# Kernel optimization log

Measured on AMD Instinct MI355X. Metric: run time of the kernel, lower is better.

The kernel has to match this reference:

```python
import jax, jax.numpy as jnp
import numpy as np

DT_SCALER = 1.0 / 24.0
ODE_STEPS = 4  # fixed-step RK4 stand-in for adaptive odeint(rtol=atol=1e-3)
B, T, D, H = 1024, 100, 32, 256
ODE_MID = 50  # hidden width of the ODE func MLP (hard-coded 50 in source)


def setup_inputs() -> dict:
    key = jax.random.key(0)
    ks = jax.random.split(key, 20)
    n = lambda k, s: jax.random.normal(k, s, dtype=jnp.float32)
    std = 0.1  # module inits weights N(0, 0.1), biases 0
    return {
        "dt": jax.random.uniform(ks[0], (B, T, 2), dtype=jnp.float32),
        "x": n(ks[1], (B, T, D)),
        # RNNCell params
        "W_ih": n(ks[2], (H, D)) * std,
        "b_ih": jnp.zeros((H,), jnp.float32),
        "W_hh": n(ks[3], (H, H)) * std,
        "b_hh": jnp.zeros((H,), jnp.float32),
        # ODE func: Linear(H,50) -> tanh -> Linear(50,H)
        "ode_w1": n(ks[4], (ODE_MID, H)) * std,
        "ode_b1": jnp.zeros((ODE_MID,), jnp.float32),
        "ode_w2": n(ks[5], (H, ODE_MID)) * std,
        "ode_b2": jnp.zeros((H,), jnp.float32),
        # mu head: l1 (H -> H//2), distribution_mu (H//2 -> 1)
        "l1_w": n(ks[6], (H // 2, H)) * std,
        "l1_b": jnp.zeros((H // 2,), jnp.float32),
        "mu_w": n(ks[7], (1, H // 2)) * std,
        "mu_b": jnp.zeros((1,), jnp.float32),
        # sigma head: Linear(H,H) -> tanh -> Linear(H,1) -> softplus
        "sig_w1": n(ks[8], (H, H)) * std,
        "sig_b1": jnp.zeros((H,), jnp.float32),
        "sig_w2": n(ks[9], (1, H)) * std,
        "sig_b2": jnp.zeros((1,), jnp.float32),
    }


def reference(dt, x, W_ih, b_ih, W_hh, b_hh, ode_w1, ode_b1, ode_w2, ode_b2,
              l1_w, l1_b, mu_w, mu_b, sig_w1, sig_b1, sig_w2, sig_b2):
    Bsz = x.shape[0]
    xs = jnp.swapaxes(x, 0, 1)                               # [T,B,D]
    dts = jnp.swapaxes(dt[:, :, 1] - dt[:, :, 0], 0, 1)[..., None]  # [T,B,1]
    h0 = jnp.zeros((Bsz, W_hh.shape[0]), x.dtype)
    hs = 1.0 / ODE_STEPS

    def ode_f(y, scale):
        # net(y) * (dt * DT_SCALER); RHS is time-independent
        return (jnp.tanh(y @ ode_w1.T + ode_b1) @ ode_w2.T + ode_b2) * scale

    def step(h, inp):
        x_i, dt_i = inp                                      # [B,D], [B,1]
        # h_t = h_t + RNNCell(x_i, h_t)
        h = h + jnp.tanh(x_i @ W_ih.T + b_ih + h @ W_hh.T + b_hh)
        scale = dt_i * DT_SCALER
        # integrate dh/dt = ode_f(h) from t=0 to t=1 (fixed-step RK4)
        def rk4(y, _):
            k1 = ode_f(y, scale)
            k2 = ode_f(y + 0.5 * hs * k1, scale)
            k3 = ode_f(y + 0.5 * hs * k2, scale)
            k4 = ode_f(y + hs * k3, scale)
            return y + (hs / 6.0) * (k1 + 2.0 * k2 + 2.0 * k3 + k4), None
        h, _ = jax.lax.scan(rk4, h, None, length=ODE_STEPS)
        # heads (eval mode: dropout is identity)
        mu = jax.nn.relu(h @ l1_w.T + l1_b) @ mu_w.T + mu_b              # [B,1]
        sig = jax.nn.softplus(jnp.tanh(h @ sig_w1.T + sig_b1) @ sig_w2.T + sig_b2)
        return h, (mu, sig)

    _, (mu_seq, sig_seq) = jax.lax.scan(step, h0, (xs, dts))
    mu_out = jnp.swapaxes(mu_seq, 0, 1)    # [B,T,1]
    sig_out = jnp.swapaxes(sig_seq, 0, 1)  # [B,T,1]
    return (mu_out, sig_out)
```

## Files before the change

kernel.cpp:

```cpp
#include <hip/hip_runtime.h>
#include <math.h>


#define NT 256

#define WS_WCAT 0
#define WS_L1P  73728
#define WS_SW1  106496
#define WS_TOT  172032

#define F4_YC   0
#define F4_MID  256
#define F4_PRR  320
#define F4_PH1  320
#define F4_PH2  1376
#define F4_XS   2416
#define F4_L1O  2448
#define F4_SG   2576
#define F4_W1   2832
#define F4_W2   6160
#define F4_END  9488
#define SM_BC   (F4_END*4)
#define SM_OB2  (SM_BC+256)
#define SM_L1B  (SM_OB2+256)
#define SM_SB1  (SM_L1B+128)
#define SM_MUW  (SM_SB1+256)
#define SM_SW2  (SM_MUW+128)
#define SM_SCL  (SM_SW2+256)
#define SM_TOTF (SM_SCL+4)
#define SMEM_BYTES (SM_TOTF*4)

__device__ __forceinline__ float fma4(float a, float4 y, float4 w) {
  a = fmaf(y.x, w.x, a); a = fmaf(y.y, w.y, a);
  a = fmaf(y.z, w.z, a); a = fmaf(y.w, w.w, a);
  return a;
}
__device__ __forceinline__ float4 add4(float4 a, float4 b) {
  return make_float4(a.x+b.x, a.y+b.y, a.z+b.z, a.w+b.w);
}
__device__ __forceinline__ float4 axpy4(float a, float4 xv, float4 yv) {
  return make_float4(fmaf(a,xv.x,yv.x), fmaf(a,xv.y,yv.y),
                     fmaf(a,xv.z,yv.z), fmaf(a,xv.w,yv.w));
}
__device__ __forceinline__ float4 muls4(float4 v, float s) {
  return make_float4(v.x*s, v.y*s, v.z*s, v.w*s);
}
__device__ __forceinline__ float tfast(float x) {
  float ax = fabsf(x);
  float e  = __expf(-2.f * ax);
  float t  = (1.f - e) * __builtin_amdgcn_rcpf(1.f + e);
  return copysignf(t, x);
}
__device__ __forceinline__ float4 tfast4(float4 v) {
  return make_float4(tfast(v.x), tfast(v.y), tfast(v.z), tfast(v.w));
}
template <int CTRL>
__device__ __forceinline__ float dpp_add(float v) {
  int s = __builtin_amdgcn_update_dpp(0, __float_as_int(v), CTRL, 0xF, 0xF, true);
  return v + __int_as_float(s);
}
__device__ __forceinline__ float red16(float v) {
  return dpp_add<0xB1>(dpp_add<0x4E>(dpp_add<0x141>(dpp_add<0x140>(v))));
}

__global__ void prep_w(const float* __restrict__ Wih, const float* __restrict__ Whh,
                       const float* __restrict__ l1w, const float* __restrict__ sw1,
                       float* __restrict__ ws) {
  int i = blockIdx.x * 256 + threadIdx.x;
  if (i < 73728) {
    int g = i >> 10, rem = i & 1023, j = rem >> 2, c = rem & 3;
    int k = 4 * g + c;
    ws[i] = (k < 32) ? Wih[j * 32 + k] : Whh[j * 256 + (k - 32)];
  } else if (i < 106496) {
    int t = i - 73728;
    int g = t >> 9, rem = t & 511, j = rem >> 2, c = rem & 3;
    ws[i] = l1w[j * 256 + 4 * g + c];
  } else if (i < WS_TOT) {
    int t = i - 106496;
    int g = t >> 10, rem = t & 1023, j = rem >> 2, c = rem & 3;
    ws[i] = sw1[j * 256 + 4 * g + c];
  }
}

__global__ __attribute__((amdgpu_flat_work_group_size(NT, NT)))
void odernn_main(const float* __restrict__ dt,
                 const float* __restrict__ x,
                 const float* __restrict__ bih,
                 const float* __restrict__ bhh,
                 const float* __restrict__ ow1,
                 const float* __restrict__ ob1g,
                 const float* __restrict__ ow2,
                 const float* __restrict__ ob2g,
                 const float* __restrict__ l1bg,
                 const float* __restrict__ muwg,
                 const float* __restrict__ mubg,
                 const float* __restrict__ sb1g,
                 const float* __restrict__ sw2g,
                 const float* __restrict__ sb2g,
                 const float* __restrict__ ws,
                 float* __restrict__ out) {
  extern __shared__ __align__(16) float sm[];
  float4* f4 = (float4*)sm;
  float* midS = sm + F4_MID * 4;
  const int tid = threadIdx.x;
  const int wv = tid >> 6, ln = tid & 63;
  const int b0 = blockIdx.x * 4;
  const bool isA = (wv & 1) == 0;
  const int ra = (wv >> 1) * 2, rb = ra + 1;

  const float4* wcat4 = (const float4*)(ws + WS_WCAT);
  const float4* l1w4  = (const float4*)(ws + WS_L1P);
  const float4* sw14  = (const float4*)(ws + WS_SW1);
  const float4* xg4   = (const float4*)x;

  for (int i = tid; i < 3328; i += NT) {
    int j = i >> 6, rem = i & 63, f = rem >> 4, kq = rem & 15;
    float4 v = make_float4(0.f, 0.f, 0.f, 0.f);
    if (j < 50) v = *(const float4*)&ow1[j * 256 + kq * 16 + 4 * f];
    f4[F4_W1 + (j * 4 + f) * 16 + kq] = v;
  }
  for (int i = tid; i < 3328; i += NT) {
    int cg = i >> 6, lq = i & 63;
    int C = cg / 13, g = cg - C * 13;
    int col = 4 * lq + C;
    float t0 = (4*g+0 < 50) ? ow2[col*50 + 4*g+0] : 0.f;
    float t1 = (4*g+1 < 50) ? ow2[col*50 + 4*g+1] : 0.f;
    float t2 = (4*g+2 < 50) ? ow2[col*50 + 4*g+2] : 0.f;
    float t3 = (4*g+3 < 50) ? ow2[col*50 + 4*g+3] : 0.f;
    f4[F4_W2 + i] = make_float4(t0, t1, t2, t3);
  }
  sm[SM_BC + tid]  = bih[tid] + bhh[tid];
  sm[SM_OB2 + tid] = ob2g[tid];
  sm[SM_SB1 + tid] = sb1g[tid];
  sm[SM_SW2 + tid] = sw2g[tid];
  if (tid < 128) { sm[SM_L1B + tid] = l1bg[tid]; sm[SM_MUW + tid] = muwg[tid]; }
  f4[F4_YC + tid] = make_float4(0.f, 0.f, 0.f, 0.f);
  if (tid < 32) {
    int r = tid >> 3, g = tid & 7;
    f4[F4_XS + tid] = xg4[((size_t)(b0 + r) * 100) * 8 + g];
  } else if (tid < 36) {
    int r = tid - 32;
    const float* dp = dt + ((size_t)(b0 + r) * 100) * 2;
    sm[SM_SCL + r] = (dp[1] - dp[0]) * (1.f / 24.f);
  }
  __syncthreads();

  const float mubv = mubg[0], sb2v = sb2g[0];
  const float4* bc4  = (const float4*)(sm + SM_BC);
  const float4* l1b4 = (const float4*)(sm + SM_L1B);
  const float4* sb14 = (const float4*)(sm + SM_SB1);
  const float4* muw4 = (const float4*)(sm + SM_MUW);
  const float4* sw24 = (const float4*)(sm + SM_SW2);

  auto RNNPART = [&]() {
    const int jq = tid & 63, kc = tid >> 6;
    float4 a0 = make_float4(0,0,0,0), a1 = a0, a2 = a0, a3 = a0;
#pragma unroll 2
    for (int gg = 0; gg < 18; ++gg) {
      int g = kc * 18 + gg;
      float4 w0 = wcat4[g * 256 + 4 * jq + 0];
      float4 w1 = wcat4[g * 256 + 4 * jq + 1];
      float4 w2 = wcat4[g * 256 + 4 * jq + 2];
      float4 w3 = wcat4[g * 256 + 4 * jq + 3];
      float4 y0 = (g < 8) ? f4[F4_XS + g]      : f4[F4_YC + (g - 8)];
      float4 y1 = (g < 8) ? f4[F4_XS + 8 + g]  : f4[F4_YC + 64 + (g - 8)];
      float4 y2 = (g < 8) ? f4[F4_XS + 16 + g] : f4[F4_YC + 128 + (g - 8)];
      float4 y3 = (g < 8) ? f4[F4_XS + 24 + g] : f4[F4_YC + 192 + (g - 8)];
      a0.x = fma4(a0.x, y0, w0); a0.y = fma4(a0.y, y0, w1);
      a0.z = fma4(a0.z, y0, w2); a0.w = fma4(a0.w, y0, w3);
      a1.x = fma4(a1.x, y1, w0); a1.y = fma4(a1.y, y1, w1);
      a1.z = fma4(a1.z, y1, w2); a1.w = fma4(a1.w, y1, w3);
      a2.x = fma4(a2.x, y2, w0); a2.y = fma4(a2.y, y2, w1);
      a2.z = fma4(a2.z, y2, w2); a2.w = fma4(a2.w, y2, w3);
      a3.x = fma4(a3.x, y3, w0); a3.y = fma4(a3.y, y3, w1);
      a3.z = fma4(a3.z, y3, w2); a3.w = fma4(a3.w, y3, w3);
    }
    f4[F4_PRR + (kc * 4 + 0) * 65 + jq] = a0;
    f4[F4_PRR + (kc * 4 + 1) * 65 + jq] = a1;
    f4[F4_PRR + (kc * 4 + 2) * 65 + jq] = a2;
    f4[F4_PRR + (kc * 4 + 3) * 65 + jq] = a3;
  };
  auto RNNRED = [&]() {
    const int r = tid >> 6, jq = tid & 63;
    float4 v = bc4[jq];
#pragma unroll
    for (int kc = 0; kc < 4; ++kc)
      v = add4(v, f4[F4_PRR + (kc * 4 + r) * 65 + jq]);
    float4 hold = f4[F4_YC + r * 64 + jq];
    f4[F4_YC + r * 64 + jq] = add4(hold, tfast4(v));
  };
  auto HEADSPART = [&]() {
    {
      const int cq = tid & 31, kc = tid >> 5;
      float4 c0 = make_float4(0,0,0,0), c1 = c0, c2 = c0, c3 = c0;
#pragma unroll 2
      for (int g = 0; g < 8; ++g) {
        int kg = kc * 8 + g;
        float4 w0 = l1w4[kg * 128 + 4 * cq + 0];
        float4 w1 = l1w4[kg * 128 + 4 * cq + 1];
        float4 w2 = l1w4[kg * 128 + 4 * cq + 2];
        float4 w3 = l1w4[kg * 128 + 4 * cq + 3];
        float4 y0 = f4[F4_YC + kg],       y1 = f4[F4_YC + 64 + kg];
        float4 y2 = f4[F4_YC + 128 + kg], y3 = f4[F4_YC + 192 + kg];
        c0.x = fma4(c0.x, y0, w0); c0.y = fma4(c0.y, y0, w1);
        c0.z = fma4(c0.z, y0, w2); c0.w = fma4(c0.w, y0, w3);
        c1.x = fma4(c1.x, y1, w0); c1.y = fma4(c1.y, y1, w1);
        c1.z = fma4(c1.z, y1, w2); c1.w = fma4(c1.w, y1, w3);
        c2.x = fma4(c2.x, y2, w0); c2.y = fma4(c2.y, y2, w1);
        c2.z = fma4(c2.z, y2, w2); c2.w = fma4(c2.w, y2, w3);
        c3.x = fma4(c3.x, y3, w0); c3.y = fma4(c3.y, y3, w1);
        c3.z = fma4(c3.z, y3, w2); c3.w = fma4(c3.w, y3, w3);
      }
      f4[F4_PH1 + (kc * 4 + 0) * 33 + cq] = c0;
      f4[F4_PH1 + (kc * 4 + 1) * 33 + cq] = c1;
      f4[F4_PH1 + (kc * 4 + 2) * 33 + cq] = c2;
      f4[F4_PH1 + (kc * 4 + 3) * 33 + cq] = c3;
    }
    {
      const int cq = tid & 63, kc = tid >> 6;
      float4 d0 = make_float4(0,0,0,0), d1 = d0, d2 = d0, d3 = d0;
#pragma unroll 2
      for (int g = 0; g < 16; ++g) {
        int kg = kc * 16 + g;
        float4 w0 = sw14[kg * 256 + 4 * cq + 0];
        float4 w1 = sw14[kg * 256 + 4 * cq + 1];
        float4 w2 = sw14[kg * 256 + 4 * cq + 2];
        float4 w3 = sw14[kg * 256 + 4 * cq + 3];
        float4 y0 = f4[F4_YC + kg],       y1 = f4[F4_YC + 64 + kg];
        float4 y2 = f4[F4_YC + 128 + kg], y3 = f4[F4_YC + 192 + kg];
        d0.x = fma4(d0.x, y0, w0); d0.y = fma4(d0.y, y0, w1);
        d0.z = fma4(d0.z, y0, w2); d0.w = fma4(d0.w, y0, w3);
        d1.x = fma4(d1.x, y1, w0); d1.y = fma4(d1.y, y1, w1);
        d1.z = fma4(d1.z, y1, w2); d1.w = fma4(d1.w, y1, w3);
        d2.x = fma4(d2.x, y2, w0); d2.y = fma4(d2.y, y2, w1);
        d2.z = fma4(d2.z, y2, w2); d2.w = fma4(d2.w, y2, w3);
        d3.x = fma4(d3.x, y3, w0); d3.y = fma4(d3.y, y3, w1);
        d3.z = fma4(d3.z, y3, w2); d3.w = fma4(d3.w, y3, w3);
      }
      f4[F4_PH2 + (kc * 4 + 0) * 65 + cq] = d0;
      f4[F4_PH2 + (kc * 4 + 1) * 65 + cq] = d1;
      f4[F4_PH2 + (kc * 4 + 2) * 65 + cq] = d2;
      f4[F4_PH2 + (kc * 4 + 3) * 65 + cq] = d3;
    }
  };
  auto HEADSRED = [&]() {
    if (tid < 128) {
      int r = tid >> 5, cq = tid & 31;
      float4 v = l1b4[cq];
#pragma unroll
      for (int kc = 0; kc < 8; ++kc)
        v = add4(v, f4[F4_PH1 + (kc * 4 + r) * 33 + cq]);
      f4[F4_L1O + r * 32 + cq] =
          make_float4(fmaxf(v.x, 0.f), fmaxf(v.y, 0.f),
                      fmaxf(v.z, 0.f), fmaxf(v.w, 0.f));
    }
    {
      int r = tid >> 6, cq = tid & 63;
      float4 v = sb14[cq];
#pragma unroll
      for (int kc = 0; kc < 4; ++kc)
        v = add4(v, f4[F4_PH2 + (kc * 4 + r) * 65 + cq]);
      f4[F4_SG + r * 64 + cq] = tfast4(v);
    }
  };
  auto DOTS = [&](int t) {
    float pm = 0.f;
    if (ln < 32) {
      float4 l = f4[F4_L1O + wv * 32 + ln];
      float4 w = muw4[ln];
      pm = l.x * w.x + l.y * w.y + l.z * w.z + l.w * w.w;
    }
#pragma unroll
    for (int off = 32; off > 0; off >>= 1) pm += __shfl_down(pm, off);
    if (ln == 0) out[(size_t)(b0 + wv) * 100 + t] = pm + mubv;
    float4 sv = f4[F4_SG + wv * 64 + ln];
    float4 w2v = sw24[ln];
    float ps = sv.x * w2v.x + sv.y * w2v.y + sv.z * w2v.z + sv.w * w2v.w;
#pragma unroll
    for (int off = 32; off > 0; off >>= 1) ps += __shfl_down(ps, off);
    if (ln == 0) {
      float z = ps + sb2v;
      float sp = fmaxf(z, 0.f) + log1pf(expf(-fabsf(z)));
      out[(size_t)102400 + (size_t)(b0 + wv) * 100 + t] = sp;
    }
  };

  if (isA) {
    const int qA = ln >> 4, kcA = ln & 15;
    float4 w1r[13][4];
    float ob1A = 0.f;
    {
      int jb = qA * 13 + kcA;
      if (kcA < 13 && jb < 50) ob1A = ob1g[jb];
    }
    auto L1 = [&](int row) {
      const float4* ycr = f4 + F4_YC + row * 64 + kcA * 4;
      float4 y0 = ycr[0], y1 = ycr[1], y2 = ycr[2], y3 = ycr[3];
      float p[13];
#pragma unroll
      for (int jj = 0; jj < 13; ++jj) {
        float s = 0.f;
        s = fma4(s, y0, w1r[jj][0]); s = fma4(s, y1, w1r[jj][1]);
        s = fma4(s, y2, w1r[jj][2]); s = fma4(s, y3, w1r[jj][3]);
        p[jj] = s;
      }
#pragma unroll
      for (int jj = 0; jj < 13; ++jj) p[jj] = red16(p[jj]);
      if (kcA < 13) {
        float v = p[0];
#pragma unroll
        for (int jj = 1; jj < 13; ++jj) v = (kcA == jj) ? p[jj] : v;
        midS[row * 64 + qA * 13 + kcA] = tfast(v + ob1A);
      }
    };

    for (int t = 0; t < 100; ++t) {
      RNNPART();  __syncthreads();
      RNNRED();   __syncthreads();
#pragma unroll
      for (int jj = 0; jj < 13; ++jj)
#pragma unroll
        for (int f = 0; f < 4; ++f)
          w1r[jj][f] = f4[F4_W1 + ((qA * 13 + jj) * 4 + f) * 16 + kcA];
#pragma unroll 1
      for (int ph = 0; ph <= 32; ++ph) {
        if (ph < 32) {
          L1(ra + (ph & 1));
        } else if (t < 99 && wv == 0) {
          if (ln < 32) {
            int r = ln >> 3, g = ln & 7;
            f4[F4_XS + ln] = xg4[((size_t)(b0 + r) * 100 + t + 1) * 8 + g];
          } else if (ln < 36) {
            int r = ln - 32;
            const float* dp = dt + ((size_t)(b0 + r) * 100 + t + 1) * 2;
            sm[SM_SCL + r] = (dp[1] - dp[0]) * (1.f / 24.f);
          }
        }
        __syncthreads();
      }
      HEADSPART(); __syncthreads();
      HEADSRED();  __syncthreads();
      DOTS(t);     __syncthreads();
    }
  } else {
    float4 w2c0[13], w2c1[13], w2c2[13], w2c3[13];
    float4 hA, hB, acA, acB;
    float sclA = 0.f, sclB = 0.f;
    auto L2 = [&](int row, int e, float4& h, float4& ac, float sc) {
      const float4* mr = (const float4*)(midS + row * 64);
      float bx = 0.f, by = 0.f, bz = 0.f, bw = 0.f;
#define L2STEP(mv, g) bx = fma4(bx, mv, w2c0[g]); by = fma4(by, mv, w2c1[g]); \
                      bz = fma4(bz, mv, w2c2[g]); bw = fma4(bw, mv, w2c3[g]);
      {
        float4 a0 = mr[0], a1 = mr[1], a2 = mr[2], a3 = mr[3], a4 = mr[4];
        L2STEP(a0, 0) L2STEP(a1, 1) L2STEP(a2, 2) L2STEP(a3, 3) L2STEP(a4, 4)
      }
      {
        float4 a0 = mr[5], a1 = mr[6], a2 = mr[7], a3 = mr[8];
        L2STEP(a0, 5) L2STEP(a1, 6) L2STEP(a2, 7) L2STEP(a3, 8)
      }
      {
        float4 a0 = mr[9], a1 = mr[10], a2 = mr[11], a3 = mr[12];
        L2STEP(a0, 9) L2STEP(a1, 10) L2STEP(a2, 11) L2STEP(a3, 12)
      }
#undef L2STEP
      float4 ob2v = ((const float4*)(sm + SM_OB2))[ln];
      float4 kv = muls4(add4(make_float4(bx, by, bz, bw), ob2v), sc);
      const int s = e & 3;
      float4 ycw;
      if (s == 0)      { ac = kv;                 ycw = axpy4(0.125f, kv, h); }
      else if (s == 1) { ac = axpy4(2.f, kv, ac); ycw = axpy4(0.125f, kv, h); }
      else if (s == 2) { ac = axpy4(2.f, kv, ac); ycw = axpy4(0.25f,  kv, h); }
      else             { h = axpy4(0.25f / 6.f, add4(ac, kv), h); ycw = h; }
      f4[F4_YC + row * 64 + ln] = ycw;
    };

    for (int t = 0; t < 100; ++t) {
      RNNPART();  __syncthreads();
      RNNRED();   __syncthreads();
#pragma unroll
      for (int g = 0; g < 13; ++g) {
        w2c0[g] = f4[F4_W2 + (0 * 13 + g) * 64 + ln];
        w2c1[g] = f4[F4_W2 + (1 * 13 + g) * 64 + ln];
        w2c2[g] = f4[F4_W2 + (2 * 13 + g) * 64 + ln];
        w2c3[g] = f4[F4_W2 + (3 * 13 + g) * 64 + ln];
      }
#pragma unroll 1
      for (int ph = 0; ph <= 32; ++ph) {
        if (ph == 0) {
          hA = f4[F4_YC + ra * 64 + ln];
          hB = f4[F4_YC + rb * 64 + ln];
          acA = make_float4(0.f, 0.f, 0.f, 0.f); acB = acA;
          sclA = sm[SM_SCL + ra]; sclB = sm[SM_SCL + rb];
        } else if (ph & 1) {
          L2(ra, (ph - 1) >> 1, hA, acA, sclA);
        } else {
          L2(rb, (ph - 2) >> 1, hB, acB, sclB);
        }
        __syncthreads();
      }
      HEADSPART(); __syncthreads();
      HEADSRED();  __syncthreads();
      DOTS(t);     __syncthreads();
    }
  }
}

extern "C" void kernel_launch(void* const* d_in, const int* in_sizes, int n_in,
                              void* d_out, int out_size, void* d_ws, size_t ws_size,
                              hipStream_t stream) {
  const float* dt  = (const float*)d_in[0];
  const float* x   = (const float*)d_in[1];
  const float* Wih = (const float*)d_in[2];
  const float* bih = (const float*)d_in[3];
  const float* Whh = (const float*)d_in[4];
  const float* bhh = (const float*)d_in[5];
  const float* ow1 = (const float*)d_in[6];
  const float* ob1 = (const float*)d_in[7];
  const float* ow2 = (const float*)d_in[8];
  const float* ob2 = (const float*)d_in[9];
  const float* l1w = (const float*)d_in[10];
  const float* l1b = (const float*)d_in[11];
  const float* muw = (const float*)d_in[12];
  const float* mub = (const float*)d_in[13];
  const float* sw1 = (const float*)d_in[14];
  const float* sb1 = (const float*)d_in[15];
  const float* sw2 = (const float*)d_in[16];
  const float* sb2 = (const float*)d_in[17];
  float* ws  = (float*)d_ws;
  float* out = (float*)d_out;

  hipFuncSetAttribute((const void*)odernn_main,
                      hipFuncAttributeMaxDynamicSharedMemorySize, SMEM_BYTES);

  prep_w<<<WS_TOT / 256, 256, 0, stream>>>(Wih, Whh, l1w, sw1, ws);
  odernn_main<<<256, NT, SMEM_BYTES, stream>>>(dt, x, bih, bhh, ow1, ob1, ow2, ob2,
                                               l1b, muw, mub, sb1, sw2, sb2, ws, out);
}
```

Before: 3.323 ms.

## Run ODE RK4 per-wave per-row without block barriers, keep W1 in registers

Drops the wave-specialized A/B split, where some waves did layer 1 and others did layer 2 with a block barrier per phase. Now each wave integrates its own batch row through all 16 RK4 stages, using only intra-wave LDS communication, so the ~33 __syncthreads per timestep go away. W1 stays in registers for the whole kernel. Intermediate state is stored in a swizzled LDS layout to avoid bank conflicts, and W2 is read from LDS on every stage. The risks are higher register pressure (waves_per_eu(1)), more LDS reads of W2, and each wave now doing both matmuls serially.

```diff
diff --git a/kernel.cpp b/kernel.cpp
--- a/kernel.cpp
+++ b/kernel.cpp
@@ -9,20 +9,19 @@
 #define WS_SW1  106496
 #define WS_TOT  172032
 
-#define F4_YC   0
-#define F4_MID  256
-#define F4_PRR  320
-#define F4_PH1  320
-#define F4_PH2  1376
-#define F4_XS   2416
-#define F4_L1O  2448
-#define F4_SG   2576
-#define F4_W1   2832
-#define F4_W2   6160
-#define F4_END  9488
+#define F4_YCT  0
+#define F4_HS   256
+#define F4_MID  512
+#define F4_PRR  576
+#define F4_PH1  576
+#define F4_PH2  1632
+#define F4_XS   2672
+#define F4_L1O  2704
+#define F4_SG   2832
+#define F4_W2   3088
+#define F4_END  6416
 #define SM_BC   (F4_END*4)
-#define SM_OB2  (SM_BC+256)
-#define SM_L1B  (SM_OB2+256)
+#define SM_L1B  (SM_BC+256)
 #define SM_SB1  (SM_L1B+128)
 #define SM_MUW  (SM_SB1+256)
 #define SM_SW2  (SM_MUW+128)
@@ -61,6 +60,9 @@
 }
 __device__ __forceinline__ float red16(float v) {
   return dpp_add<0xB1>(dpp_add<0x4E>(dpp_add<0x141>(dpp_add<0x140>(v))));
+}
+__device__ __forceinline__ int ycphys(int a) {
+  return ((a & 3) << 4) + ((a >> 2) ^ (a & 3));
 }
 
 __global__ void prep_w(const float* __restrict__ Wih, const float* __restrict__ Whh,
@@ -83,6 +85,7 @@
 }
 
 __global__ __attribute__((amdgpu_flat_work_group_size(NT, NT)))
+__attribute__((amdgpu_waves_per_eu(1)))
 void odernn_main(const float* __restrict__ dt,
                  const float* __restrict__ x,
                  const float* __restrict__ bih,
@@ -105,20 +108,27 @@
   const int tid = threadIdx.x;
   const int wv = tid >> 6, ln = tid & 63;
   const int b0 = blockIdx.x * 4;
-  const bool isA = (wv & 1) == 0;
-  const int ra = (wv >> 1) * 2, rb = ra + 1;
 
   const float4* wcat4 = (const float4*)(ws + WS_WCAT);
   const float4* l1w4  = (const float4*)(ws + WS_L1P);
   const float4* sw14  = (const float4*)(ws + WS_SW1);
   const float4* xg4   = (const float4*)x;
 
-  for (int i = tid; i < 3328; i += NT) {
-    int j = i >> 6, rem = i & 63, f = rem >> 4, kq = rem & 15;
-    float4 v = make_float4(0.f, 0.f, 0.f, 0.f);
-    if (j < 50) v = *(const float4*)&ow1[j * 256 + kq * 16 + 4 * f];
-    f4[F4_W1 + (j * 4 + f) * 16 + kq] = v;
-  }
+  const int qA = ln >> 4, kcA = ln & 15;
+  float4 w1r[13][4];
+  float  ob1r[13];
+#pragma unroll
+  for (int jj = 0; jj < 13; ++jj) {
+    int j = qA * 13 + jj;
+    ob1r[jj] = (j < 50) ? ob1g[j] : 0.f;
+#pragma unroll
+    for (int f = 0; f < 4; ++f)
+      w1r[jj][f] = (j < 50)
+          ? *(const float4*)&ow1[j * 256 + kcA * 16 + 4 * f]
+          : make_float4(0.f, 0.f, 0.f, 0.f);
+  }
+  float4 ob2r = *(const float4*)&ob2g[4 * ln];
+
   for (int i = tid; i < 3328; i += NT) {
     int cg = i >> 6, lq = i & 63;
     int C = cg / 13, g = cg - C * 13;
@@ -129,12 +139,11 @@
     float t3 = (4*g+3 < 50) ? ow2[col*50 + 4*g+3] : 0.f;
     f4[F4_W2 + i] = make_float4(t0, t1, t2, t3);
   }
-  sm[SM_BC + tid]  = bih[tid] + bhh[tid];
-  sm[SM_OB2 + tid] = ob2g[tid];
+  sm[SM_BC + tid] = bih[tid] + bhh[tid];
   sm[SM_SB1 + tid] = sb1g[tid];
   sm[SM_SW2 + tid] = sw2g[tid];
   if (tid < 128) { sm[SM_L1B + tid] = l1bg[tid]; sm[SM_MUW + tid] = muwg[tid]; }
-  f4[F4_YC + tid] = make_float4(0.f, 0.f, 0.f, 0.f);
+  f4[F4_HS + tid] = make_float4(0.f, 0.f, 0.f, 0.f);
   if (tid < 32) {
     int r = tid >> 3, g = tid & 7;
     f4[F4_XS + tid] = xg4[((size_t)(b0 + r) * 100) * 8 + g];
@@ -151,45 +160,94 @@
   const float4* sb14 = (const float4*)(sm + SM_SB1);
   const float4* muw4 = (const float4*)(sm + SM_MUW);
   const float4* sw24 = (const float4*)(sm + SM_SW2);
-
-  auto RNNPART = [&]() {
-    const int jq = tid & 63, kc = tid >> 6;
-    float4 a0 = make_float4(0,0,0,0), a1 = a0, a2 = a0, a3 = a0;
+  const float4* mid4 = (const float4*)midS;
+
+  const int physW = ycphys(ln);
+  const int rowb = wv * 64;
+
+  for (int t = 0; t < 100; ++t) {
+    {
+      const int jq = tid & 63, kc = tid >> 6;
+      float4 a0 = make_float4(0,0,0,0), a1 = a0, a2 = a0, a3 = a0;
 #pragma unroll 2
-    for (int gg = 0; gg < 18; ++gg) {
-      int g = kc * 18 + gg;
-      float4 w0 = wcat4[g * 256 + 4 * jq + 0];
-      float4 w1 = wcat4[g * 256 + 4 * jq + 1];
-      float4 w2 = wcat4[g * 256 + 4 * jq + 2];
-      float4 w3 = wcat4[g * 256 + 4 * jq + 3];
-      float4 y0 = (g < 8) ? f4[F4_XS + g]      : f4[F4_YC + (g - 8)];
-      float4 y1 = (g < 8) ? f4[F4_XS + 8 + g]  : f4[F4_YC + 64 + (g - 8)];
-      float4 y2 = (g < 8) ? f4[F4_XS + 16 + g] : f4[F4_YC + 128 + (g - 8)];
-      float4 y3 = (g < 8) ? f4[F4_XS + 24 + g] : f4[F4_YC + 192 + (g - 8)];
-      a0.x = fma4(a0.x, y0, w0); a0.y = fma4(a0.y, y0, w1);
-      a0.z = fma4(a0.z, y0, w2); a0.w = fma4(a0.w, y0, w3);
-      a1.x = fma4(a1.x, y1, w0); a1.y = fma4(a1.y, y1, w1);
-      a1.z = fma4(a1.z, y1, w2); a1.w = fma4(a1.w, y1, w3);
-      a2.x = fma4(a2.x, y2, w0); a2.y = fma4(a2.y, y2, w1);
-      a2.z = fma4(a2.z, y2, w2); a2.w = fma4(a2.w, y2, w3);
-      a3.x = fma4(a3.x, y3, w0); a3.y = fma4(a3.y, y3, w1);
-      a3.z = fma4(a3.z, y3, w2); a3.w = fma4(a3.w, y3, w3);
-    }
-    f4[F4_PRR + (kc * 4 + 0) * 65 + jq] = a0;
-    f4[F4_PRR + (kc * 4 + 1) * 65 + jq] = a1;
-    f4[F4_PRR + (kc * 4 + 2) * 65 + jq] = a2;
-    f4[F4_PRR + (kc * 4 + 3) * 65 + jq] = a3;
-  };
-  auto RNNRED = [&]() {
-    const int r = tid >> 6, jq = tid & 63;
-    float4 v = bc4[jq];
-#pragma unroll
-    for (int kc = 0; kc < 4; ++kc)
-      v = add4(v, f4[F4_PRR + (kc * 4 + r) * 65 + jq]);
-    float4 hold = f4[F4_YC + r * 64 + jq];
-    f4[F4_YC + r * 64 + jq] = add4(hold, tfast4(v));
-  };
-  auto HEADSPART = [&]() {
+      for (int gg = 0; gg < 18; ++gg) {
+        int g = kc * 18 + gg;
+        float4 w0 = wcat4[g * 256 + 4 * jq + 0];
+        float4 w1 = wcat4[g * 256 + 4 * jq + 1];
+        float4 w2 = wcat4[g * 256 + 4 * jq + 2];
+        float4 w3 = wcat4[g * 256 + 4 * jq + 3];
+        float4 y0 = (g < 8) ? f4[F4_XS + g]      : f4[F4_HS + (g - 8)];
+        float4 y1 = (g < 8) ? f4[F4_XS + 8 + g]  : f4[F4_HS + 64 + (g - 8)];
+        float4 y2 = (g < 8) ? f4[F4_XS + 16 + g] : f4[F4_HS + 128 + (g - 8)];
+        float4 y3 = (g < 8) ? f4[F4_XS + 24 + g] : f4[F4_HS + 192 + (g - 8)];
+        a0.x = fma4(a0.x, y0, w0); a0.y = fma4(a0.y, y0, w1);
+        a0.z = fma4(a0.z, y0, w2); a0.w = fma4(a0.w, y0, w3);
+        a1.x = fma4(a1.x, y1, w0); a1.y = fma4(a1.y, y1, w1);
+        a1.z = fma4(a1.z, y1, w2); a1.w = fma4(a1.w, y1, w3);
+        a2.x = fma4(a2.x, y2, w0); a2.y = fma4(a2.y, y2, w1);
+        a2.z = fma4(a2.z, y2, w2); a2.w = fma4(a2.w, y2, w3);
+        a3.x = fma4(a3.x, y3, w0); a3.y = fma4(a3.y, y3, w1);
+        a3.z = fma4(a3.z, y3, w2); a3.w = fma4(a3.w, y3, w3);
+      }
+      f4[F4_PRR + (kc * 4 + 0) * 65 + jq] = a0;
+      f4[F4_PRR + (kc * 4 + 1) * 65 + jq] = a1;
+      f4[F4_PRR + (kc * 4 + 2) * 65 + jq] = a2;
+      f4[F4_PRR + (kc * 4 + 3) * 65 + jq] = a3;
+    }
+    __syncthreads();
+    float4 h;
+    {
+      float4 v = bc4[ln];
+#pragma unroll
+      for (int kc = 0; kc < 4; ++kc)
+        v = add4(v, f4[F4_PRR + (kc * 4 + wv) * 65 + ln]);
+      h = add4(f4[F4_HS + rowb + ln], tfast4(v));
+      f4[F4_YCT + rowb + physW] = h;
+    }
+    float4 ac = make_float4(0.f, 0.f, 0.f, 0.f);
+    const float sc = sm[SM_SCL + wv];
+#pragma unroll 1
+    for (int e = 0; e < 16; ++e) {
+      float4 y0 = f4[F4_YCT + rowb + 0 * 16 + (kcA ^ 0)];
+      float4 y1 = f4[F4_YCT + rowb + 1 * 16 + (kcA ^ 1)];
+      float4 y2 = f4[F4_YCT + rowb + 2 * 16 + (kcA ^ 2)];
+      float4 y3 = f4[F4_YCT + rowb + 3 * 16 + (kcA ^ 3)];
+      float p[13];
+#pragma unroll
+      for (int jj = 0; jj < 13; ++jj) {
+        float s = 0.f;
+        s = fma4(s, y0, w1r[jj][0]); s = fma4(s, y1, w1r[jj][1]);
+        s = fma4(s, y2, w1r[jj][2]); s = fma4(s, y3, w1r[jj][3]);
+        p[jj] = s;
+      }
+#pragma unroll
+      for (int jj = 0; jj < 13; ++jj) p[jj] = red16(p[jj]);
+      if (kcA == 0) {
+#pragma unroll
+        for (int jj = 0; jj < 13; ++jj)
+          midS[wv * 64 + qA * 13 + jj] = tfast(p[jj] + ob1r[jj]);
+      }
+      float bx = 0.f, by = 0.f, bz = 0.f, bw = 0.f;
+#pragma unroll
+      for (int g = 0; g < 13; ++g) {
+        float4 m = mid4[wv * 16 + g];
+        bx = fma4(bx, m, f4[F4_W2 + (0 * 13 + g) * 64 + ln]);
+        by = fma4(by, m, f4[F4_W2 + (1 * 13 + g) * 64 + ln]);
+        bz = fma4(bz, m, f4[F4_W2 + (2 * 13 + g) * 64 + ln]);
+        bw = fma4(bw, m, f4[F4_W2 + (3 * 13 + g) * 64 + ln]);
+      }
+      float4 kv = muls4(add4(make_float4(bx, by, bz, bw), ob2r), sc);
+      const int s = e & 3;
+      float4 ycw;
+      if (s == 0)      { ac = kv;                 ycw = axpy4(0.125f, kv, h); }
+      else if (s == 1) { ac = axpy4(2.f, kv, ac); ycw = axpy4(0.125f, kv, h); }
+      else if (s == 2) { ac = axpy4(2.f, kv, ac); ycw = axpy4(0.25f,  kv, h); }
+      else             { h = axpy4(0.25f / 6.f, add4(ac, kv), h); ycw = h; }
+      f4[F4_YCT + rowb + physW] = ycw;
+    }
+    f4[F4_HS + rowb + ln] = h;
+    __syncthreads();
+
     {
       const int cq = tid & 31, kc = tid >> 5;
       float4 c0 = make_float4(0,0,0,0), c1 = c0, c2 = c0, c3 = c0;
@@ -200,8 +258,8 @@
         float4 w1 = l1w4[kg * 128 + 4 * cq + 1];
         float4 w2 = l1w4[kg * 128 + 4 * cq + 2];
         float4 w3 = l1w4[kg * 128 + 4 * cq + 3];
-        float4 y0 = f4[F4_YC + kg],       y1 = f4[F4_YC + 64 + kg];
-        float4 y2 = f4[F4_YC + 128 + kg], y3 = f4[F4_YC + 192 + kg];
+        float4 y0 = f4[F4_HS + kg],       y1 = f4[F4_HS + 64 + kg];
+        float4 y2 = f4[F4_HS + 128 + kg], y3 = f4[F4_HS + 192 + kg];
         c0.x = fma4(c0.x, y0, w0); c0.y = fma4(c0.y, y0, w1);
         c0.z = fma4(c0.z, y0, w2); c0.w = fma4(c0.w, y0, w3);
         c1.x = fma4(c1.x, y1, w0); c1.y = fma4(c1.y, y1, w1);
@@ -226,8 +284,8 @@
         float4 w1 = sw14[kg * 256 + 4 * cq + 1];
         float4 w2 = sw14[kg * 256 + 4 * cq + 2];
         float4 w3 = sw14[kg * 256 + 4 * cq + 3];
-        float4 y0 = f4[F4_YC + kg],       y1 = f4[F4_YC + 64 + kg];
-        float4 y2 = f4[F4_YC + 128 + kg], y3 = f4[F4_YC + 192 + kg];
+        float4 y0 = f4[F4_HS + kg],       y1 = f4[F4_HS + 64 + kg];
+        float4 y2 = f4[F4_HS + 128 + kg], y3 = f4[F4_HS + 192 + kg];
         d0.x = fma4(d0.x, y0, w0); d0.y = fma4(d0.y, y0, w1);
         d0.z = fma4(d0.z, y0, w2); d0.w = fma4(d0.w, y0, w3);
         d1.x = fma4(d1.x, y1, w0); d1.y = fma4(d1.y, y1, w1);
@@ -242,8 +300,17 @@
       f4[F4_PH2 + (kc * 4 + 2) * 65 + cq] = d2;
       f4[F4_PH2 + (kc * 4 + 3) * 65 + cq] = d3;
     }
-  };
-  auto HEADSRED = [&]() {
+    if (t < 99) {
+      if (tid < 32) {
+        int r = tid >> 3, g = tid & 7;
+        f4[F4_XS + tid] = xg4[((size_t)(b0 + r) * 100 + t + 1) * 8 + g];
+      } else if (tid < 36) {
+        int r = tid - 32;
+        const float* dp = dt + ((size_t)(b0 + r) * 100 + t + 1) * 2;
+        sm[SM_SCL + r] = (dp[1] - dp[0]) * (1.f / 24.f);
+      }
+    }
+    __syncthreads();
     if (tid < 128) {
       int r = tid >> 5, cq = tid & 31;
       float4 v = l1b4[cq];
@@ -262,146 +329,27 @@
         v = add4(v, f4[F4_PH2 + (kc * 4 + r) * 65 + cq]);
       f4[F4_SG + r * 64 + cq] = tfast4(v);
     }
-  };
-  auto DOTS = [&](int t) {
-    float pm = 0.f;
-    if (ln < 32) {
-      float4 l = f4[F4_L1O + wv * 32 + ln];
-      float4 w = muw4[ln];
-      pm = l.x * w.x + l.y * w.y + l.z * w.z + l.w * w.w;
-    }
-#pragma unroll
-    for (int off = 32; off > 0; off >>= 1) pm += __shfl_down(pm, off);
-    if (ln == 0) out[(size_t)(b0 + wv) * 100 + t] = pm + mubv;
-    float4 sv = f4[F4_SG + wv * 64 + ln];
-    float4 w2v = sw24[ln];
-    float ps = sv.x * w2v.x + sv.y * w2v.y + sv.z * w2v.z + sv.w * w2v.w;
-#pragma unroll
-    for (int off = 32; off > 0; off >>= 1) ps += __shfl_down(ps, off);
-    if (ln == 0) {
-      float z = ps + sb2v;
-      float sp = fmaxf(z, 0.f) + log1pf(expf(-fabsf(z)));
-      out[(size_t)102400 + (size_t)(b0 + wv) * 100 + t] = sp;
-    }
-  };
-
-  if (isA) {
-    const int qA = ln >> 4, kcA = ln & 15;
-    float4 w1r[13][4];
-    float ob1A = 0.f;
-    {
-      int jb = qA * 13 + kcA;
-      if (kcA < 13 && jb < 50) ob1A = ob1g[jb];
-    }
-    auto L1 = [&](int row) {
-      const float4* ycr = f4 + F4_YC + row * 64 + kcA * 4;
-      float4 y0 = ycr[0], y1 = ycr[1], y2 = ycr[2], y3 = ycr[3];
-      float p[13];
-#pragma unroll
-      for (int jj = 0; jj < 13; ++jj) {
-        float s = 0.f;
-        s = fma4(s, y0, w1r[jj][0]); s = fma4(s, y1, w1r[jj][1]);
-        s = fma4(s, y2, w1r[jj][2]); s = fma4(s, y3, w1r[jj][3]);
-        p[jj] = s;
-      }
-#pragma unroll
-      for (int jj = 0; jj < 13; ++jj) p[jj] = red16(p[jj]);
-      if (kcA < 13) {
-        float v = p[0];
-#pragma unroll
-        for (int jj = 1; jj < 13; ++jj) v = (kcA == jj) ? p[jj] : v;
-        midS[row * 64 + qA * 13 + kcA] = tfast(v + ob1A);
-      }
-    };
-
-    for (int t = 0; t < 100; ++t) {
-      RNNPART();  __syncthreads();
-      RNNRED();   __syncthreads();
-#pragma unroll
-      for (int jj = 0; jj < 13; ++jj)
-#pragma unroll
-        for (int f = 0; f < 4; ++f)
-          w1r[jj][f] = f4[F4_W1 + ((qA * 13 + jj) * 4 + f) * 16 + kcA];
-#pragma unroll 1
-      for (int ph = 0; ph <= 32; ++ph) {
-        if (ph < 32) {
-          L1(ra + (ph & 1));
-        } else if (t < 99 && wv == 0) {
-          if (ln < 32) {
-            int r = ln >> 3, g = ln & 7;
-            f4[F4_XS + ln] = xg4[((size_t)(b0 + r) * 100 + t + 1) * 8 + g];
-          } else if (ln < 36) {
-            int r = ln - 32;
-            const float* dp = dt + ((size_t)(b0 + r) * 100 + t + 1) * 2;
-            sm[SM_SCL + r] = (dp[1] - dp[0]) * (1.f / 24.f);
-          }
-        }
-        __syncthreads();
-      }
-      HEADSPART(); __syncthreads();
-      HEADSRED();  __syncthreads();
-      DOTS(t);     __syncthreads();
-    }
-  } else {
-    float4 w2c0[13], w2c1[13], w2c2[13], w2c3[13];
-    float4 hA, hB, acA, acB;
-    float sclA = 0.f, sclB = 0.f;
-    auto L2 = [&](int row, int e, float4& h, float4& ac, float sc) {
-      const float4* mr = (const float4*)(midS + row * 64);
-      float bx = 0.f, by = 0.f, bz = 0.f, bw = 0.f;
-#define L2STEP(mv, g) bx = fma4(bx, mv, w2c0[g]); by = fma4(by, mv, w2c1[g]); \
-                      bz = fma4(bz, mv, w2c2[g]); bw = fma4(bw, mv, w2c3[g]);
-      {
-        float4 a0 = mr[0], a1 = mr[1], a2 = mr[2], a3 = mr[3], a4 = mr[4];
-        L2STEP(a0, 0) L2STEP(a1, 1) L2STEP(a2, 2) L2STEP(a3, 3) L2STEP(a4, 4)
-      }
-      {
-        float4 a0 = mr[5], a1 = mr[6], a2 = mr[7], a3 = mr[8];
-        L2STEP(a0, 5) L2STEP(a1, 6) L2STEP(a2, 7) L2STEP(a3, 8)
-      }
-      {
-        float4 a0 = mr[9], a1 = mr[10], a2 = mr[11], a3 = mr[12];
-        L2STEP(a0, 9) L2STEP(a1, 10) L2STEP(a2, 11) L2STEP(a3, 12)
-      }
-#undef L2STEP
-      float4 ob2v = ((const float4*)(sm + SM_OB2))[ln];
-      float4 kv = muls4(add4(make_float4(bx, by, bz, bw), ob2v), sc);
-      const int s = e & 3;
-      float4 ycw;
-      if (s == 0)      { ac = kv;                 ycw = axpy4(0.125f, kv, h); }
-      else if (s == 1) { ac = axpy4(2.f, kv, ac); ycw = axpy4(0.125f, kv, h); }
-      else if (s == 2) { ac = axpy4(2.f, kv, ac); ycw = axpy4(0.25f,  kv, h); }
-      else             { h = axpy4(0.25f / 6.f, add4(ac, kv), h); ycw = h; }
-      f4[F4_YC + row * 64 + ln] = ycw;
-    };
-
-    for (int t = 0; t < 100; ++t) {
-      RNNPART();  __syncthreads();
-      RNNRED();   __syncthreads();
-#pragma unroll
-      for (int g = 0; g < 13; ++g) {
-        w2c0[g] = f4[F4_W2 + (0 * 13 + g) * 64 + ln];
-        w2c1[g] = f4[F4_W2 + (1 * 13 + g) * 64 + ln];
-        w2c2[g] = f4[F4_W2 + (2 * 13 + g) * 64 + ln];
-        w2c3[g] = f4[F4_W2 + (3 * 13 + g) * 64 + ln];
-      }
-#pragma unroll 1
-      for (int ph = 0; ph <= 32; ++ph) {
-        if (ph == 0) {
-          hA = f4[F4_YC + ra * 64 + ln];
-          hB = f4[F4_YC + rb * 64 + ln];
-          acA = make_float4(0.f, 0.f, 0.f, 0.f); acB = acA;
-          sclA = sm[SM_SCL + ra]; sclB = sm[SM_SCL + rb];
-        } else if (ph & 1) {
-          L2(ra, (ph - 1) >> 1, hA, acA, sclA);
-        } else {
-          L2(rb, (ph - 2) >> 1, hB, acB, sclB);
-        }
-        __syncthreads();
-      }
-      HEADSPART(); __syncthreads();
-      HEADSRED();  __syncthreads();
-      DOTS(t);     __syncthreads();
+    __syncthreads();
+    {
+      float pm = 0.f;
+      if (ln < 32) {
+        float4 l = f4[F4_L1O + wv * 32 + ln];
+        float4 w = muw4[ln];
+        pm = l.x * w.x + l.y * w.y + l.z * w.z + l.w * w.w;
+      }
+#pragma unroll
+      for (int off = 32; off > 0; off >>= 1) pm += __shfl_down(pm, off);
+      if (ln == 0) out[(size_t)(b0 + wv) * 100 + t] = pm + mubv;
+      float4 sv = f4[F4_SG + wv * 64 + ln];
+      float4 w2v = sw24[ln];
+      float ps = sv.x * w2v.x + sv.y * w2v.y + sv.z * w2v.z + sv.w * w2v.w;
+#pragma unroll
+      for (int off = 32; off > 0; off >>= 1) ps += __shfl_down(ps, off);
+      if (ln == 0) {
+        float z = ps + sb2v;
+        float sp = fmaxf(z, 0.f) + log1pf(expf(-fabsf(z)));
+        out[(size_t)102400 + (size_t)(b0 + wv) * 100 + t] = sp;
+      }
     }
   }
 }
```

After: 4.750 ms. 1.43x slower.
